# Kernel tuning notes

Hardware: AMD Instinct MI355X
Metric: run time of the kernel (lower is better)

The kernel has to match this reference:

```python
import jax, jax.numpy as jnp
import numpy as np

PATCH_GRID = 28          # _embed hard-codes reshape(28, 28, D)
TARGET_HW = (224, 224)   # input_shape[-2:] for RescaleSegmentor


def setup_inputs() -> dict:
    key = jax.random.key(0)
    k1, k2 = jax.random.split(key)
    B = 8
    D = 1536          # 768 (CLS) + 768 (patch token) concat from DINO vitb8
    N_BANK = 50000    # coreset memory bank size
    features = jax.random.normal(k1, (B * PATCH_GRID * PATCH_GRID, D), dtype=jnp.float32)
    memory_bank = jax.random.normal(k2, (N_BANK, D), dtype=jnp.float32)
    return {"features": features, "memory_bank": memory_bank, "batchsize": B}


def reference(features, memory_bank, batchsize):
    # FaissNN IndexFlatL2 with k=1: min squared-L2 distance per query.
    # d2[i,j] = ||q_i||^2 + ||b_j||^2 - 2 q_i . b_j
    qn = jnp.sum(features * features, axis=-1, keepdims=True)          # [Q,1]
    bn = jnp.sum(memory_bank * memory_bank, axis=-1)                   # [N]
    d2 = qn + bn[None, :] - 2.0 * (features @ memory_bank.T)           # [Q,N]
    patch_scores = jnp.min(d2, axis=-1)                                # [Q] (k=1 -> mean of 1 NN)
    # unpatch_scores + PatchMaker.score: max over patches per image
    patch_maps = patch_scores.reshape(batchsize, PATCH_GRID, PATCH_GRID)
    image_scores = jnp.max(patch_maps.reshape(batchsize, -1), axis=-1)  # [B]
    # RescaleSegmentor: bilinear upsample of patch score map to input size
    masks = jax.image.resize(
        patch_maps, (batchsize, TARGET_HW[0], TARGET_HW[1]), method="linear"
    )
    return image_scores, masks
```

## Files before the change

### kernel.cpp

```cpp
#include <hip/hip_runtime.h>
#include <stdint.h>

#define DIM   1536
#define NQ    6272
#define NQP   6400
#define NB    50000
#define NBP2  50176
#define MT2   25
#define NT2   196
#define GRID2 (MT2 * NT2)
#define NKT   24
#define NIT   12
#define NPIX  (8 * 224 * 224)

typedef float f32x4 __attribute__((ext_vector_type(4)));
typedef int   i32x4 __attribute__((ext_vector_type(4)));
typedef __attribute__((address_space(3))) signed char lds_i8;

__device__ inline void gll16(const signed char* g, signed char* l) {
  __builtin_amdgcn_global_load_lds(
      (const __attribute__((address_space(1))) uint32_t*)g,
      (__attribute__((address_space(3))) uint32_t*)l, 16, 0, 0);
}

__global__ void init_kernel(uint32_t* __restrict__ minbits, float* __restrict__ out_scores) {
  int i = blockIdx.x * 256 + threadIdx.x;
  if (i < NQP) minbits[i] = 0x7F800000u;
  if (i < 8)   out_scores[i] = 0.0f;
}

__global__ void quant_rows(const float* __restrict__ src, signed char* __restrict__ dst,
                           float* __restrict__ norms, float* __restrict__ scales,
                           int nsrc, int ndst) {
  int row  = blockIdx.x * 4 + (threadIdx.x >> 6);
  int lane = threadIdx.x & 63;
  if (row >= ndst) return;
  uint32_t* drow = (uint32_t*)(dst + (size_t)row * DIM);
  if (row < nsrc) {
    const float4* s = (const float4*)(src + (size_t)row * DIM);
    float4 v[6]; float ns = 0.f, mx = 0.f;
#pragma unroll
    for (int i = 0; i < 6; ++i) {
      v[i] = s[lane + 64 * i];
      ns += v[i].x * v[i].x + v[i].y * v[i].y + v[i].z * v[i].z + v[i].w * v[i].w;
      mx = fmaxf(mx, fmaxf(fmaxf(fabsf(v[i].x), fabsf(v[i].y)),
                           fmaxf(fabsf(v[i].z), fabsf(v[i].w))));
    }
#pragma unroll
    for (int off = 32; off >= 1; off >>= 1) {
      ns += __shfl_xor(ns, off);
      mx = fmaxf(mx, __shfl_xor(mx, off));
    }
    float inv = (mx > 0.f) ? 127.0f / mx : 0.f;
#pragma unroll
    for (int i = 0; i < 6; ++i) {
      int a = max(-127, min(127, __float2int_rn(v[i].x * inv)));
      int b = max(-127, min(127, __float2int_rn(v[i].y * inv)));
      int c = max(-127, min(127, __float2int_rn(v[i].z * inv)));
      int d = max(-127, min(127, __float2int_rn(v[i].w * inv)));
      drow[lane + 64 * i] = (uint32_t)(a & 255) | ((uint32_t)(b & 255) << 8) |
                            ((uint32_t)(c & 255) << 16) | ((uint32_t)(d & 255) << 24);
    }
    if (lane == 0) { norms[row] = ns; scales[row] = mx * (1.0f / 127.0f); }
  } else {
#pragma unroll
    for (int i = 0; i < 6; ++i) drow[lane + 64 * i] = 0u;
    if (lane == 0) { norms[row] = 1e30f; scales[row] = 0.f; }
  }
}

#define BAR   do { asm volatile("s_barrier" ::: "memory"); \
                   __builtin_amdgcn_sched_barrier(0); } while(0)
#define LGKM(n) do { asm volatile("s_waitcnt lgkmcnt(" #n ")" ::: "memory"); \
                     __builtin_amdgcn_sched_barrier(0); } while(0)
#define VM0   asm volatile("s_waitcnt vmcnt(0)" ::: "memory")
#define VM2   asm volatile("s_waitcnt vmcnt(2)" ::: "memory")
#define PHI   __builtin_amdgcn_s_setprio(1)
#define PLO   __builtin_amdgcn_s_setprio(0)

#define DSR(dst, base, imm) \
  asm volatile("ds_read_b128 %0, %1 offset:%2" : "=v"(dst) : "v"(base), "i"(imm))

#define RD_A2(dst, i0, bufI, frag) do { \
  DSR(dst[i0],       aOff, (bufI) * 16384 + (frag) * 1024);       \
  DSR(dst[(i0) + 1], aOff, (bufI) * 16384 + ((frag) + 1) * 1024); \
} while(0)

#define RD_B2(dst, i0, bufI, frag) do { \
  DSR(dst[i0],       bOff, (bufI) * 16384 + (frag) * 1024);       \
  DSR(dst[(i0) + 1], bOff, (bufI) * 16384 + ((frag) + 1) * 1024); \
} while(0)

#define MFMA8(mb, x0, x1, b4) do { \
  _Pragma("unroll") for (int n_ = 0; n_ < 4; ++n_) { \
    acc[(mb)][n_]     = __builtin_amdgcn_mfma_i32_16x16x64_i8( \
      __builtin_bit_cast(i32x4, (x0)), __builtin_bit_cast(i32x4, b4[n_]), acc[(mb)][n_], 0, 0, 0); \
    acc[(mb) + 1][n_] = __builtin_amdgcn_mfma_i32_16x16x64_i8( \
      __builtin_bit_cast(i32x4, (x1)), __builtin_bit_cast(i32x4, b4[n_]), acc[(mb) + 1][n_], 0, 0, 0); \
  } \
} while(0)

#define STAGE_A(bufI, ktc) do { \
  const signed char* _g = gA + (size_t)srow * DIM + (ktc) + scol; \
  gll16(_g,                      &sA[bufI][sdst]); \
  gll16(_g + (size_t)128 * DIM,  &sA[bufI][8192 + sdst]); \
} while(0)

#define STAGE_B(bufI, ktc) do { \
  const signed char* _g = gB + (size_t)srow * DIM + (ktc) + scol; \
  gll16(_g,                      &sB[bufI][sdst]); \
  gll16(_g + (size_t)128 * DIM,  &sB[bufI][8192 + sdst]); \
} while(0)

#define ITER(T0, SN, TAIL) do { \
   RD_A2(aQ, 0, 0, 4); RD_B2(bO, 0, 1, 0); \
    LGKM(6); BAR; PHI; MFMA8(0, aP[0], aP[1], bE); PLO; \
   RD_A2(aQ, 2, 0, 6); RD_B2(bO, 2, 1, 2); \
    LGKM(8); \
    if (SN) { STAGE_B(0, (T0) + 128); VM2; } else { VM0; } \
    BAR; PHI; MFMA8(2, aP[2], aP[3], bE); PLO; \
   RD_A2(aP, 0, 1, 0); \
    LGKM(2); BAR; PHI; MFMA8(4, aQ[0], aQ[1], bE); PLO; \
   RD_A2(aP, 2, 1, 2); \
    LGKM(4); \
    if (SN) { STAGE_A(0, (T0) + 128); VM2; } \
    BAR; PHI; MFMA8(6, aQ[2], aQ[3], bE); PLO; \
   RD_A2(aQ, 0, 1, 4); \
    if (!TAIL) { RD_B2(bE, 0, 0, 0); LGKM(6); } else { LGKM(4); } \
    BAR; PHI; MFMA8(0, aP[0], aP[1], bO); PLO; \
   RD_A2(aQ, 2, 1, 6); \
    if (!TAIL) { RD_B2(bE, 2, 0, 2); LGKM(8); } else { LGKM(4); } \
    if (SN) { STAGE_B(1, (T0) + 192); VM2; } \
    BAR; PHI; MFMA8(2, aP[2], aP[3], bO); PLO; \
   if (!TAIL) { RD_A2(aP, 0, 0, 0); } \
    LGKM(2); BAR; PHI; MFMA8(4, aQ[0], aQ[1], bO); PLO; \
   if (!TAIL) { RD_A2(aP, 2, 0, 2); LGKM(4); } else { LGKM(0); } \
    if (SN) { STAGE_A(1, (T0) + 192); VM2; } \
    BAR; PHI; MFMA8(6, aQ[2], aQ[3], bO); PLO; \
} while(0)

__global__ __launch_bounds__(512, 2)
void gemm_min8(const signed char* __restrict__ fA, const signed char* __restrict__ bB,
               const float* __restrict__ bn, const float* __restrict__ bscale,
               const float* __restrict__ qscale, uint32_t* __restrict__ minbits) {
  __shared__ __align__(16) signed char sA[2][16384];
  __shared__ __align__(16) signed char sB[2][16384];

  const int nwg = GRID2;
  int bid = blockIdx.x;
  const int qch = nwg >> 3, rch = nwg & 7;
  int xcd = bid & 7, loc = bid >> 3;
  int swz = (xcd < rch ? xcd * (qch + 1) : rch * (qch + 1) + (xcd - rch) * qch) + loc;
  int mt = swz % MT2;
  int nt = swz / MT2;

  int tid = threadIdx.x;
  int lane = tid & 63, wave = tid >> 6;
  int wm = wave >> 2, wn = wave & 3, bq = wn & 1, bh = wn >> 1;
  int lr = lane & 15, k16 = lane >> 4;

  const signed char* gA = fA + (size_t)(mt * 256) * DIM;
  const signed char* gB = bB + (size_t)(nt * 256) * DIM;

  int srow = tid >> 2;
  int scol = ((tid & 3) ^ ((tid >> 3) & 3)) * 16;
  int sdst = tid * 16;

  int cxA = (k16 ^ ((lr >> 1) & 3)) * 16;
  uint32_t aOff = (uint32_t)(uintptr_t)(lds_i8*)&sA[0][(wm * 128 + lr) * 64 + cxA];
  uint32_t bOff = (uint32_t)(uintptr_t)(lds_i8*)&sB[0][(bh * 128 + bq * 64 + lr) * 64 + cxA];

  i32x4 acc[8][4] = {};
  f32x4 aP[4], aQ[4], bE[4], bO[4];

  STAGE_A(0, 0); STAGE_B(0, 0);
  STAGE_B(1, 64); STAGE_A(1, 64);
  VM2; BAR;
  RD_B2(bE, 0, 0, 0); RD_B2(bE, 2, 0, 2);
  RD_A2(aP, 0, 0, 0); RD_A2(aP, 2, 0, 2);

#pragma unroll 1
  for (int i = 0; i < NIT - 1; ++i) {
    ITER(i * 128, 1, 0);
  }
  ITER((NIT - 1) * 128, 0, 1);

  float bnv[4], bsv[4];
#pragma unroll
  for (int n_ = 0; n_ < 4; ++n_) {
    int col = nt * 256 + wn * 64 + n_ * 16 + lr;
    bnv[n_] = bn[col];
    bsv[n_] = 2.0f * bscale[col];
  }
  int qbase = mt * 256 + wm * 128;
#pragma unroll
  for (int m_ = 0; m_ < 8; ++m_) {
    f32x4 sq = *(const f32x4*)&qscale[qbase + m_ * 16 + (lane >> 4) * 4];
#pragma unroll
    for (int r = 0; r < 4; ++r) {
      float sqr = sq[r];
      float v =          bnv[0] - bsv[0] * sqr * (float)acc[m_][0][r];
      v = fminf(v, bnv[1] - bsv[1] * sqr * (float)acc[m_][1][r]);
      v = fminf(v, bnv[2] - bsv[2] * sqr * (float)acc[m_][2][r]);
      v = fminf(v, bnv[3] - bsv[3] * sqr * (float)acc[m_][3][r]);
      v = fminf(v, __shfl_xor(v, 1));
      v = fminf(v, __shfl_xor(v, 2));
      v = fminf(v, __shfl_xor(v, 4));
      v = fminf(v, __shfl_xor(v, 8));
      if (lr == 0) {
        int q = qbase + m_ * 16 + (lane >> 4) * 4 + r;
        atomicMin(&minbits[q], __float_as_uint(v));
      }
    }
  }
}

__global__ void scores_kernel(const uint32_t* __restrict__ minbits, const float* __restrict__ qn,
                              float* __restrict__ ps, float* __restrict__ img) {
  int q = blockIdx.x * 256 + threadIdx.x;
  if (q >= NQ) return;
  float s = __uint_as_float(minbits[q]) + qn[q];
  ps[q] = s;
  atomicMax((uint32_t*)&img[q / 784], __float_as_uint(s));
}

__global__ void resize_kernel(const float* __restrict__ ps, float* __restrict__ masks) {
  int idx = blockIdx.x * 256 + threadIdx.x;
  if (idx >= NPIX) return;
  int b   = idx / (224 * 224);
  int rem = idx - b * (224 * 224);
  int oy  = rem / 224;
  int ox  = rem - oy * 224;
  float sy = (oy + 0.5f) * 0.125f - 0.5f;
  float sx = (ox + 0.5f) * 0.125f - 0.5f;
  float fy0 = floorf(sy), fx0 = floorf(sx);
  int y0 = (int)fy0, x0 = (int)fx0;
  float fy = sy - fy0, fx = sx - fx0;
  int y0c = min(max(y0, 0), 27),     y1c = min(max(y0 + 1, 0), 27);
  int x0c = min(max(x0, 0), 27),     x1c = min(max(x0 + 1, 0), 27);
  const float* p = ps + b * 784;
  float top = p[y0c * 28 + x0c] * (1.f - fx) + p[y0c * 28 + x1c] * fx;
  float bot = p[y1c * 28 + x0c] * (1.f - fx) + p[y1c * 28 + x1c] * fx;
  masks[idx] = top * (1.f - fy) + bot * fy;
}

extern "C" void kernel_launch(void* const* d_in, const int* in_sizes, int n_in,
                              void* d_out, int out_size, void* d_ws, size_t ws_size,
                              hipStream_t stream) {
  const float* features = (const float*)d_in[0];
  const float* bank     = (const float*)d_in[1];

  char* ws = (char*)d_ws;
  size_t off = 0;
  signed char* bankQ = (signed char*)(ws + off); off += (size_t)NBP2 * DIM;
  signed char* featQ = (signed char*)(ws + off); off += (size_t)NQP * DIM;
  float*    bn      = (float*)(ws + off);    off += (size_t)NBP2 * 4;
  float*    qn      = (float*)(ws + off);    off += (size_t)NQP * 4;
  float*    bscale  = (float*)(ws + off);    off += (size_t)NBP2 * 4;
  float*    qscale  = (float*)(ws + off);    off += (size_t)NQP * 4;
  uint32_t* minbits = (uint32_t*)(ws + off); off += (size_t)NQP * 4;
  float*    ps      = (float*)(ws + off);    off += (size_t)NQ * 4;

  float* out_scores = (float*)d_out;
  float* masks      = out_scores + 8;

  hipLaunchKernelGGL(init_kernel, dim3(25), dim3(256), 0, stream, minbits, out_scores);
  hipLaunchKernelGGL(quant_rows, dim3(NBP2 / 4), dim3(256), 0, stream, bank, bankQ, bn, bscale, NB, NBP2);
  hipLaunchKernelGGL(quant_rows, dim3(NQP / 4), dim3(256), 0, stream, features, featQ, qn, qscale, NQ, NQP);
  hipLaunchKernelGGL(gemm_min8, dim3(GRID2), dim3(512), 0, stream, featQ, bankQ, bn, bscale, qscale, minbits);
  hipLaunchKernelGGL(scores_kernel, dim3(25), dim3(256), 0, stream, minbits, qn, ps, out_scores);
  hipLaunchKernelGGL(resize_kernel, dim3((NPIX + 255) / 256), dim3(256), 0, stream, ps, masks);
}
```

Baseline: 701.3 us.

## Restructure int8 GEMM main loop into four larger MFMA phases per iteration

Reworks the software-pipelined K loop of the int8 distance GEMM. Each iteration now has four phases of 16 MFMAs instead of eight phases of 8, with LDS fragment reads batched four at a time and an extra register buffer (aQ0) holding the second A half. Global-to-LDS staging is regrouped around the new phase boundaries. The goal is fewer barriers and wait points per K step; the cost is more live registers under 512x2 launch bounds and a more delicate ordering of waits and staging.

```diff
diff --git a/kernel.cpp b/kernel.cpp
--- a/kernel.cpp
+++ b/kernel.cpp
@@ -81,23 +81,26 @@
 #define DSR(dst, base, imm) \
   asm volatile("ds_read_b128 %0, %1 offset:%2" : "=v"(dst) : "v"(base), "i"(imm))
 
-#define RD_A2(dst, i0, bufI, frag) do { \
-  DSR(dst[i0],       aOff, (bufI) * 16384 + (frag) * 1024);       \
-  DSR(dst[(i0) + 1], aOff, (bufI) * 16384 + ((frag) + 1) * 1024); \
-} while(0)
-
-#define RD_B2(dst, i0, bufI, frag) do { \
-  DSR(dst[i0],       bOff, (bufI) * 16384 + (frag) * 1024);       \
-  DSR(dst[(i0) + 1], bOff, (bufI) * 16384 + ((frag) + 1) * 1024); \
-} while(0)
-
-#define MFMA8(mb, x0, x1, b4) do { \
-  _Pragma("unroll") for (int n_ = 0; n_ < 4; ++n_) { \
-    acc[(mb)][n_]     = __builtin_amdgcn_mfma_i32_16x16x64_i8( \
-      __builtin_bit_cast(i32x4, (x0)), __builtin_bit_cast(i32x4, b4[n_]), acc[(mb)][n_], 0, 0, 0); \
-    acc[(mb) + 1][n_] = __builtin_amdgcn_mfma_i32_16x16x64_i8( \
-      __builtin_bit_cast(i32x4, (x1)), __builtin_bit_cast(i32x4, b4[n_]), acc[(mb) + 1][n_], 0, 0, 0); \
-  } \
+#define RD_A4(dst, bufI, frag) do { \
+  DSR(dst[0], aOff, (bufI) * 16384 + ((frag) + 0) * 1024); \
+  DSR(dst[1], aOff, (bufI) * 16384 + ((frag) + 1) * 1024); \
+  DSR(dst[2], aOff, (bufI) * 16384 + ((frag) + 2) * 1024); \
+  DSR(dst[3], aOff, (bufI) * 16384 + ((frag) + 3) * 1024); \
+} while(0)
+
+#define RD_B4(dst, bufI) do { \
+  DSR(dst[0], bOff, (bufI) * 16384 + 0);    \
+  DSR(dst[1], bOff, (bufI) * 16384 + 1024); \
+  DSR(dst[2], bOff, (bufI) * 16384 + 2048); \
+  DSR(dst[3], bOff, (bufI) * 16384 + 3072); \
+} while(0)
+
+#define MFMA16(mb, a4, b4) do { \
+  _Pragma("unroll") for (int m_ = 0; m_ < 4; ++m_) \
+  _Pragma("unroll") for (int n_ = 0; n_ < 4; ++n_) \
+    acc[(mb) + m_][n_] = __builtin_amdgcn_mfma_i32_16x16x64_i8( \
+      __builtin_bit_cast(i32x4, a4[m_]), __builtin_bit_cast(i32x4, b4[n_]), \
+      acc[(mb) + m_][n_], 0, 0, 0); \
 } while(0)
 
 #define STAGE_A(bufI, ktc) do { \
@@ -113,30 +116,20 @@
 } while(0)
 
 #define ITER(T0, SN, TAIL) do { \
-   RD_A2(aQ, 0, 0, 4); RD_B2(bO, 0, 1, 0); \
-    LGKM(6); BAR; PHI; MFMA8(0, aP[0], aP[1], bE); PLO; \
-   RD_A2(aQ, 2, 0, 6); RD_B2(bO, 2, 1, 2); \
+   RD_A4(aQ, 0, 4); RD_B4(bO, 1); \
     LGKM(8); \
     if (SN) { STAGE_B(0, (T0) + 128); VM2; } else { VM0; } \
-    BAR; PHI; MFMA8(2, aP[2], aP[3], bE); PLO; \
-   RD_A2(aP, 0, 1, 0); \
-    LGKM(2); BAR; PHI; MFMA8(4, aQ[0], aQ[1], bE); PLO; \
-   RD_A2(aP, 2, 1, 2); \
+    BAR; PHI; MFMA16(0, aP, bE); PLO; \
+   RD_A4(aP, 1, 0); RD_A4(aQ, 1, 4); \
+    LGKM(8); if (SN) { VM0; } \
+    BAR; PHI; MFMA16(4, aQ0, bE); PLO; \
+   if (!TAIL) { RD_B4(bE, 0); } \
     LGKM(4); \
-    if (SN) { STAGE_A(0, (T0) + 128); VM2; } \
-    BAR; PHI; MFMA8(6, aQ[2], aQ[3], bE); PLO; \
-   RD_A2(aQ, 0, 1, 4); \
-    if (!TAIL) { RD_B2(bE, 0, 0, 0); LGKM(6); } else { LGKM(4); } \
-    BAR; PHI; MFMA8(0, aP[0], aP[1], bO); PLO; \
-   RD_A2(aQ, 2, 1, 6); \
-    if (!TAIL) { RD_B2(bE, 2, 0, 2); LGKM(8); } else { LGKM(4); } \
-    if (SN) { STAGE_B(1, (T0) + 192); VM2; } \
-    BAR; PHI; MFMA8(2, aP[2], aP[3], bO); PLO; \
-   if (!TAIL) { RD_A2(aP, 0, 0, 0); } \
-    LGKM(2); BAR; PHI; MFMA8(4, aQ[0], aQ[1], bO); PLO; \
-   if (!TAIL) { RD_A2(aP, 2, 0, 2); LGKM(4); } else { LGKM(0); } \
+    if (SN) { STAGE_A(0, (T0) + 128); STAGE_B(1, (T0) + 192); VM2; } \
+    BAR; PHI; MFMA16(0, aP, bO); PLO; \
+   if (!TAIL) { RD_A4(aP, 0, 0); LGKM(8); } else { LGKM(0); } \
     if (SN) { STAGE_A(1, (T0) + 192); VM2; } \
-    BAR; PHI; MFMA8(6, aQ[2], aQ[3], bO); PLO; \
+    BAR; PHI; MFMA16(4, aQ, bO); PLO; \
 } while(0)
 
 __global__ __launch_bounds__(512, 2)
@@ -172,18 +165,48 @@
 
   i32x4 acc[8][4] = {};
   f32x4 aP[4], aQ[4], bE[4], bO[4];
+  f32x4 aQ0[4];
+
+#define RD_A4Q0() do { \
+  DSR(aQ0[0], aOff, 0 * 16384 + 4 * 1024); DSR(aQ0[1], aOff, 0 * 16384 + 5 * 1024); \
+  DSR(aQ0[2], aOff, 0 * 16384 + 6 * 1024); DSR(aQ0[3], aOff, 0 * 16384 + 7 * 1024); \
+} while(0)
 
   STAGE_A(0, 0); STAGE_B(0, 0);
   STAGE_B(1, 64); STAGE_A(1, 64);
   VM2; BAR;
-  RD_B2(bE, 0, 0, 0); RD_B2(bE, 2, 0, 2);
-  RD_A2(aP, 0, 0, 0); RD_A2(aP, 2, 0, 2);
+  RD_A4(aP, 0, 0); RD_B4(bE, 0);
 
 #pragma unroll 1
   for (int i = 0; i < NIT - 1; ++i) {
-    ITER(i * 128, 1, 0);
-  }
-  ITER((NIT - 1) * 128, 0, 1);
+    int T0 = i * 128;
+     RD_A4Q0(); RD_B4(bO, 1);
+      LGKM(8);
+      STAGE_B(0, T0 + 128); VM2;
+      BAR; PHI; MFMA16(0, aP, bE); PLO;
+     RD_A4(aP, 1, 0); RD_A4(aQ, 1, 4);
+      LGKM(8); VM0;
+      BAR; PHI; MFMA16(4, aQ0, bE); PLO;
+     RD_B4(bE, 0);
+      LGKM(4);
+      STAGE_A(0, T0 + 128); STAGE_B(1, T0 + 192); VM2;
+      BAR; PHI; MFMA16(0, aP, bO); PLO;
+     RD_A4(aP, 0, 0); LGKM(8);
+      STAGE_A(1, T0 + 192); VM2;
+      BAR; PHI; MFMA16(4, aQ, bO); PLO;
+  }
+  {
+     RD_A4Q0(); RD_B4(bO, 1);
+      LGKM(8); VM0;
+      BAR; PHI; MFMA16(0, aP, bE); PLO;
+     RD_A4(aP, 1, 0); RD_A4(aQ, 1, 4);
+      LGKM(8);
+      BAR; PHI; MFMA16(4, aQ0, bE); PLO;
+     LGKM(4);
+      BAR; PHI; MFMA16(0, aP, bO); PLO;
+     LGKM(0);
+      BAR; PHI; MFMA16(4, aQ, bO); PLO;
+  }
 
   float bnv[4], bsv[4];
 #pragma unroll
```

Result: slower. 783.1 us (+11.7%).
